# Kernel tuning notes

Hardware: AMD Instinct MI355X
Metric: run time of the kernel (lower is better)

Reference implementation:

```python
import jax, jax.numpy as jnp
import numpy as np

B = 4096      # batch
N = 32768     # total tree nodes (real + pseudo classes) = columns of x
L = 12        # tree path depth (levels)
K = 64        # siblings (brother nodes) per level, padded to fixed width
C = 16384     # number of real classes (range of y)


def setup_inputs() -> dict:
    key = jax.random.key(0)
    k1, k2, k3, k4 = jax.random.split(key, 4)
    x = jax.random.normal(k1, (B, N), dtype=jnp.float32)
    # per-level sibling index sets (constants derived from the cover tree /
    # new2index / index2brother dicts in the original module)
    brother = jax.random.randint(k2, (L, K), 0, N)
    # the true path node at each level must be one of that level's siblings
    pos = jax.random.randint(k3, (L,), 0, K)
    p_y = brother[jnp.arange(L), pos]
    y = jax.random.randint(k4, (B,), 0, C)  # class labels (path selection baked into brother/p_y)
    return {"x": x, "brother": brother, "p_y": p_y, "y": y}


def reference(x, brother, p_y, y):
    # x: [B, N] logits over all tree nodes; brother: [L, K]; p_y: [L]
    gathered = x[:, brother]                      # [B, L, K] irregular column gather
    logp = jax.nn.log_softmax(gathered, axis=-1)  # per-level softmax over siblings
    # label = first position of the path node within its sibling set (torch nonzero()[0])
    labels = jnp.argmax(brother == p_y[:, None], axis=-1)          # [L]
    sel = jnp.take_along_axis(logp, labels[None, :, None], axis=2)[..., 0]  # [B, L]
    # CrossEntropyLoss = mean over batch of NLL, summed across tree levels
    return (-sel).mean(axis=0).sum()
```

## Files before the change

### kernel.cpp

```cpp
#include <hip/hip_runtime.h>

#define BB 4096
#define NN 32768
#define LL 12
#define KK 64
#define SS (LL * KK)

constexpr int TPB    = 256;
constexpr int NBLK   = 2048;
constexpr int RPB    = BB / NBLK;
constexpr int F4_ROW = NN / 4;
constexpr int F4_THR = F4_ROW / TPB;
constexpr int UNROLL = 8;

constexpr size_t WS_MAP  = 0;
constexpr size_t WS_DUP  = 65536;
constexpr size_t WS_PART = 69632;

__global__ __launch_bounds__(256) void build_map(
    const int* __restrict__ brother,
    short* __restrict__ map,
    short* __restrict__ dup) {
    for (int i = threadIdx.x; i < NN * 2 / 8; i += TPB)
        ((unsigned long long*)map)[i] = 0ULL;
    __syncthreads();
    for (int s = threadIdx.x; s < SS; s += TPB)
        map[brother[s]] = (short)(s + 1);
    __syncthreads();
    for (int s = threadIdx.x; s < SS; s += TPB)
        dup[s] = (short)(map[brother[s]] - 1);
}

__global__ __launch_bounds__(256) void hsm_stream(
    const float* __restrict__ x,
    const int* __restrict__ brother,
    const int* __restrict__ p_y,
    const short* __restrict__ map,
    const short* __restrict__ dupv,
    float* __restrict__ partials) {

    __shared__ float gath[SS];

    const int w    = threadIdx.x >> 6;
    const int lane = threadIdx.x & 63;

    int dslot[3], label[3];
    #pragma unroll
    for (int j = 0; j < 3; ++j) {
        const int l   = w + 4 * j;
        const int col = brother[l * KK + lane];
        const int py  = p_y[l];
        label[j] = __ffsll(__ballot(col == py)) - 1;
        dslot[j] = dupv[l * KK + lane];
    }
    float acc[3] = {0.f, 0.f, 0.f};

    const uint2* mp = (const uint2*)map;

    for (int r = 0; r < RPB; ++r) {
        const int b = blockIdx.x * RPB + r;
        const float4* __restrict__ xr = (const float4*)(x + (size_t)b * NN);

        #pragma unroll 1
        for (int base = 0; base < F4_THR; base += UNROLL) {
            float4 v[UNROLL];
            uint2  m[UNROLL];
            #pragma unroll
            for (int u = 0; u < UNROLL; ++u) {
                const int fi = (base + u) * TPB + threadIdx.x;
                v[u] = xr[fi];
                m[u] = mp[fi];
            }
            #pragma unroll
            for (int u = 0; u < UNROLL; ++u) {
                if (m[u].x | m[u].y) {
                    const int s0 = (int)(short)(m[u].x & 0xffff);
                    const int s1 = (int)(short)(m[u].x >> 16);
                    const int s2 = (int)(short)(m[u].y & 0xffff);
                    const int s3 = (int)(short)(m[u].y >> 16);
                    if (s0 > 0) gath[s0 - 1] = v[u].x;
                    if (s1 > 0) gath[s1 - 1] = v[u].y;
                    if (s2 > 0) gath[s2 - 1] = v[u].z;
                    if (s3 > 0) gath[s3 - 1] = v[u].w;
                }
            }
        }
        __syncthreads();

        #pragma unroll
        for (int j = 0; j < 3; ++j) {
            const float vv = gath[dslot[j]];
            float mx = vv;
            #pragma unroll
            for (int o = 32; o > 0; o >>= 1) mx = fmaxf(mx, __shfl_xor(mx, o));
            float s = __expf(vv - mx);
            #pragma unroll
            for (int o = 32; o > 0; o >>= 1) s += __shfl_xor(s, o);
            acc[j] += mx + __logf(s) - __shfl(vv, label[j]);
        }
        __syncthreads();
    }

    if (lane == 0) {
        #pragma unroll
        for (int j = 0; j < 3; ++j)
            partials[(w + 4 * j) * NBLK + blockIdx.x] = acc[j];
    }
}

__global__ __launch_bounds__(256) void hsm_final(
    const float* __restrict__ partials, float* __restrict__ out) {
    const int w = threadIdx.x >> 6, lane = threadIdx.x & 63;
    __shared__ float red[LL];
    #pragma unroll
    for (int j = 0; j < 3; ++j) {
        const int l = w + 4 * j;
        float s = 0.f;
        for (int i = lane; i < NBLK; i += 64) s += partials[l * NBLK + i];
        #pragma unroll
        for (int o = 32; o > 0; o >>= 1) s += __shfl_xor(s, o);
        if (lane == 0) red[l] = s / (float)BB;
    }
    __syncthreads();
    if (threadIdx.x == 0) {
        float t = 0.f;
        #pragma unroll
        for (int i = 0; i < LL; ++i) t += red[i];
        out[0] = t;
    }
}

extern "C" void kernel_launch(void* const* d_in, const int* in_sizes, int n_in,
                              void* d_out, int out_size, void* d_ws, size_t ws_size,
                              hipStream_t stream) {
    const float* x       = (const float*)d_in[0];
    const int*   brother = (const int*)d_in[1];
    const int*   p_y     = (const int*)d_in[2];
    float* out = (float*)d_out;
    char*  ws  = (char*)d_ws;

    short* map      = (short*)(ws + WS_MAP);
    short* dup      = (short*)(ws + WS_DUP);
    float* partials = (float*)(ws + WS_PART);

    build_map<<<1, TPB, 0, stream>>>(brother, map, dup);
    hsm_stream<<<NBLK, TPB, 0, stream>>>(x, brother, p_y, map, dup, partials);
    hsm_final<<<1, 256, 0, stream>>>(partials, out);
}
```

Baseline: 713.0 us.

## Replace global slot map with per-block shared bitmap and prefix-sum compaction

Drops the separate build_map kernel and the per-element 16-bit slot map read from global memory. Each block now builds a 32768-bit presence bitmap of the sibling columns in shared memory and a prefix count per word. Scattered elements are compacted into the gather buffer by popcount rank. The row stream is software-pipelined with double-buffered float4 batches, prefetching the next row while the current one scatters, and the grid is halved to 1024 blocks with 4 rows each. The intent is to stop streaming an extra 64 KB map per row on top of x. The cost is per-block bitmap construction, atomics and more registers.

```diff
diff --git a/kernel.cpp b/kernel.cpp
--- a/kernel.cpp
+++ b/kernel.cpp
@@ -6,85 +6,104 @@
 #define KK 64
 #define SS (LL * KK)
 
-constexpr int TPB    = 256;
-constexpr int NBLK   = 2048;
-constexpr int RPB    = BB / NBLK;
-constexpr int F4_ROW = NN / 4;
-constexpr int F4_THR = F4_ROW / TPB;
-constexpr int UNROLL = 8;
+constexpr int TPB   = 256;
+constexpr int NBLK  = 1024;
+constexpr int RPB   = BB / NBLK;
+constexpr int F4ROW = NN / 4;
+constexpr int BATCH = 8;
+constexpr int NWRD  = NN / 32;
 
-constexpr size_t WS_MAP  = 0;
-constexpr size_t WS_DUP  = 65536;
-constexpr size_t WS_PART = 69632;
+#define LOADB(dst, rowp, bt) do {                                   \
+    _Pragma("unroll")                                               \
+    for (int u = 0; u < BATCH; ++u)                                 \
+        dst[u] = (rowp)[((bt) * BATCH + u) * TPB + tid];            \
+} while (0)
 
-__global__ __launch_bounds__(256) void build_map(
-    const int* __restrict__ brother,
-    short* __restrict__ map,
-    short* __restrict__ dup) {
-    for (int i = threadIdx.x; i < NN * 2 / 8; i += TPB)
-        ((unsigned long long*)map)[i] = 0ULL;
-    __syncthreads();
-    for (int s = threadIdx.x; s < SS; s += TPB)
-        map[brother[s]] = (short)(s + 1);
-    __syncthreads();
-    for (int s = threadIdx.x; s < SS; s += TPB)
-        dup[s] = (short)(map[brother[s]] - 1);
-}
+#define SCAT(src, bt) do {                                          \
+    _Pragma("unroll")                                               \
+    for (int u = 0; u < BATCH; ++u) {                               \
+        const int fi = ((bt) * BATCH + u) * TPB + tid;              \
+        const int wi = fi >> 3;                                     \
+        const unsigned wrd = bmp[wi];                               \
+        const int sh = (fi & 7) << 2;                               \
+        const unsigned nib = (wrd >> sh) & 0xFu;                    \
+        if (nib) {                                                  \
+            int r = pfx[wi] + __popc(wrd & ((1u << sh) - 1u));      \
+            if (nib & 1u) gath[r++] = src[u].x;                     \
+            if (nib & 2u) gath[r++] = src[u].y;                     \
+            if (nib & 4u) gath[r++] = src[u].z;                     \
+            if (nib & 8u) gath[r++] = src[u].w;                     \
+        }                                                           \
+    }                                                               \
+} while (0)
 
-__global__ __launch_bounds__(256) void hsm_stream(
+__global__ __launch_bounds__(TPB) void hsm_stream(
     const float* __restrict__ x,
     const int* __restrict__ brother,
     const int* __restrict__ p_y,
-    const short* __restrict__ map,
-    const short* __restrict__ dupv,
     float* __restrict__ partials) {
 
-    __shared__ float gath[SS];
+    __shared__ unsigned bmp[NWRD];
+    __shared__ int      pfx[NWRD];
+    __shared__ float    gath[SS];
 
-    const int w    = threadIdx.x >> 6;
-    const int lane = threadIdx.x & 63;
+    const int tid  = threadIdx.x;
+    const int w    = tid >> 6;
+    const int lane = tid & 63;
 
-    int dslot[3], label[3];
+    const float4* xr = (const float4*)(x + (size_t)(blockIdx.x * RPB) * NN);
+    float4 va[BATCH], vb[BATCH];
+    LOADB(va, xr, 0);
+
+    #pragma unroll
+    for (int i = 0; i < NWRD / TPB; ++i) bmp[i * TPB + tid] = 0u;
+    __syncthreads();
+
+    int cols[3], label[3];
     #pragma unroll
     for (int j = 0; j < 3; ++j) {
-        const int l   = w + 4 * j;
-        const int col = brother[l * KK + lane];
-        const int py  = p_y[l];
-        label[j] = __ffsll(__ballot(col == py)) - 1;
-        dslot[j] = dupv[l * KK + lane];
+        const int l = w + 4 * j;
+        cols[j] = brother[l * KK + lane];
+        label[j] = __ffsll(__ballot(cols[j] == p_y[l])) - 1;
+        const int s = j * TPB + tid;
+        atomicOr(&bmp[brother[s] >> 5], 1u << (brother[s] & 31));
+    }
+    __syncthreads();
+
+    if (tid < 64) {
+        int carry = 0;
+        for (int c = 0; c < NWRD / 64; ++c) {
+            const int v = __popc(bmp[c * 64 + tid]);
+            int inc = v;
+            #pragma unroll
+            for (int o = 1; o < 64; o <<= 1) {
+                const int t = __shfl_up(inc, o);
+                if (tid >= o) inc += t;
+            }
+            pfx[c * 64 + tid] = carry + inc - v;
+            carry += __shfl(inc, 63);
+        }
+    }
+    __syncthreads();
+
+    int dslot[3];
+    #pragma unroll
+    for (int j = 0; j < 3; ++j) {
+        const int c = cols[j];
+        dslot[j] = pfx[c >> 5] + __popc(bmp[c >> 5] & ((1u << (c & 31)) - 1u));
     }
     float acc[3] = {0.f, 0.f, 0.f};
 
-    const uint2* mp = (const uint2*)map;
-
     for (int r = 0; r < RPB; ++r) {
-        const int b = blockIdx.x * RPB + r;
-        const float4* __restrict__ xr = (const float4*)(x + (size_t)b * NN);
-
-        #pragma unroll 1
-        for (int base = 0; base < F4_THR; base += UNROLL) {
-            float4 v[UNROLL];
-            uint2  m[UNROLL];
-            #pragma unroll
-            for (int u = 0; u < UNROLL; ++u) {
-                const int fi = (base + u) * TPB + threadIdx.x;
-                v[u] = xr[fi];
-                m[u] = mp[fi];
-            }
-            #pragma unroll
-            for (int u = 0; u < UNROLL; ++u) {
-                if (m[u].x | m[u].y) {
-                    const int s0 = (int)(short)(m[u].x & 0xffff);
-                    const int s1 = (int)(short)(m[u].x >> 16);
-                    const int s2 = (int)(short)(m[u].y & 0xffff);
-                    const int s3 = (int)(short)(m[u].y >> 16);
-                    if (s0 > 0) gath[s0 - 1] = v[u].x;
-                    if (s1 > 0) gath[s1 - 1] = v[u].y;
-                    if (s2 > 0) gath[s2 - 1] = v[u].z;
-                    if (s3 > 0) gath[s3 - 1] = v[u].w;
-                }
-            }
-        }
+        LOADB(vb, xr, 1);
+        SCAT(va, 0);
+        LOADB(va, xr, 2);
+        SCAT(vb, 1);
+        LOADB(vb, xr, 3);
+        SCAT(va, 2);
+        const float4* xn = xr + F4ROW;
+        if (r + 1 < RPB) LOADB(va, xn, 0);
+        SCAT(vb, 3);
         __syncthreads();
 
         #pragma unroll
@@ -99,6 +118,7 @@
             acc[j] += mx + __logf(s) - __shfl(vv, label[j]);
         }
         __syncthreads();
+        xr = xn;
     }
 
     if (lane == 0) {
@@ -136,14 +156,9 @@
     const float* x       = (const float*)d_in[0];
     const int*   brother = (const int*)d_in[1];
     const int*   p_y     = (const int*)d_in[2];
-    float* out = (float*)d_out;
-    char*  ws  = (char*)d_ws;
+    float* out      = (float*)d_out;
+    float* partials = (float*)d_ws;
 
-    short* map      = (short*)(ws + WS_MAP);
-    short* dup      = (short*)(ws + WS_DUP);
-    float* partials = (float*)(ws + WS_PART);
-
-    build_map<<<1, TPB, 0, stream>>>(brother, map, dup);
-    hsm_stream<<<NBLK, TPB, 0, stream>>>(x, brother, p_y, map, dup, partials);
+    hsm_stream<<<NBLK, TPB, 0, stream>>>(x, brother, p_y, partials);
     hsm_final<<<1, 256, 0, stream>>>(partials, out);
 }
```

New measurement: 695.8 us. 2.4% less time.
